# Performance work log

Measured on AMD Instinct MI355X. Metric: run time of the kernel, lower is better.

Reference implementation:

```python
import jax, jax.numpy as jnp
import numpy as np

NUM_LEVELS = 1000
DIMENSIONS = 10000


def setup_inputs() -> dict:
    key = jax.random.key(0)
    k1, k2, k3, k4 = jax.random.split(key, 4)
    x = jax.random.uniform(k1, (32, 1, 28, 28), dtype=jnp.float32)  # MNIST-like, values in [0,1)
    # torchhd Random / Level hypervectors are +/-1 (MAP VSA)
    pos_weight = jnp.where(jax.random.normal(k2, (784, DIMENSIONS)) > 0, 1.0, -1.0).astype(jnp.float32)
    level_weight = jnp.where(jax.random.normal(k3, (NUM_LEVELS, DIMENSIONS)) > 0, 1.0, -1.0).astype(jnp.float32)
    classify_weight = jax.random.normal(k4, (10, DIMENSIONS), dtype=jnp.float32) * 0.01
    return {"x": x, "pos_weight": pos_weight, "level_weight": level_weight,
            "classify_weight": classify_weight}


def reference(x, pos_weight, level_weight, classify_weight):
    B = x.shape[0]
    xf = x.reshape(B, -1)  # flatten -> [B, 784]
    # Level embedding: quantize value in [0,1] to nearest of NUM_LEVELS indices
    idx = jnp.clip(jnp.round(xf * (NUM_LEVELS - 1)), 0, NUM_LEVELS - 1).astype(jnp.int32)
    levels = jnp.take(level_weight, idx, axis=0)  # [B, 784, D] gather
    # bind (elementwise mult with position HVs) + multiset (sum over pixels)
    hv = jnp.einsum('pd,bpd->bd', pos_weight, levels)  # [B, D]
    # hard_quantize: sign with 0 -> -1
    enc = jnp.where(hv > 0, 1.0, -1.0).astype(hv.dtype)
    logit = enc @ classify_weight.T  # [B, num_classes]
    return logit
```

## Files before the change

### kernel.cpp

```cpp
#include <hip/hip_runtime.h>
#include <stdint.h>

#define D    10000
#define P    784
#define B    32
#define NL   1000
#define NC   10

#define ROWW 320
#define ROWB (ROWW * 4)
#define NW   313
#define CHUNKS 8
#define PLEN  98
#define PLANES 7

#define OFFS_OFF  0
#define LVL_OFF   (B * P * 4)
#define POS_OFF   (LVL_OFF + NL * ROWB)
#define PART_OFF  (POS_OFF + P * ROWB)

#define PACK_BPR 10

__global__ void k_pack(const float* __restrict__ x,
                       const float* __restrict__ lvl, const float* __restrict__ pos,
                       int* __restrict__ offs,
                       uint32_t* __restrict__ lvl_b, uint32_t* __restrict__ pos_b) {
    int bx  = blockIdx.x;
    int row = bx / PACK_BPR;
    int seg = bx % PACK_BPR;
    int d0  = seg * 1024 + threadIdx.x * 4;
    const float* src; uint32_t* dst;
    if (row < NL) { src = lvl + (size_t)row * D;        dst = lvl_b + (size_t)row * ROWW; }
    else          { src = pos + (size_t)(row - NL) * D; dst = pos_b + (size_t)(row - NL) * ROWW; }

    uint32_t nib = 0;
    if (d0 < D) {
        float4 v = *(const float4*)(src + d0);
        nib = (v.x < 0.0f ? 1u : 0u) | (v.y < 0.0f ? 2u : 0u) |
              (v.z < 0.0f ? 4u : 0u) | (v.w < 0.0f ? 8u : 0u);
    }
    int lane = threadIdx.x & 63;
    uint32_t val = nib << ((lane & 7) * 4);
    val |= __shfl_xor(val, 1, 64);
    val |= __shfl_xor(val, 2, 64);
    val |= __shfl_xor(val, 4, 64);
    if ((lane & 7) == 0) {
        int gword = (seg * 1024 + (threadIdx.x & ~7) * 4) >> 5;
        dst[gword] = val;
    }

    if (bx < 98) {
        int i = bx * 256 + threadIdx.x;
        float v = rintf(x[i] * 999.0f);
        v = fminf(fmaxf(v, 0.0f), 999.0f);
        offs[i] = (int)v * ROWB;
    }
}

__global__ __launch_bounds__(64) void k_bind(const int* __restrict__ offs,
                                             const uint32_t* __restrict__ lvl_b,
                                             const uint32_t* __restrict__ pos_b,
                                             uint32_t* __restrict__ part) {
    int b = blockIdx.z, c = blockIdx.y;
    int w = blockIdx.x * 64 + threadIdx.x;
    const int* po = offs + b * P + c * PLEN;
    const uint32_t* pb = pos_b + (size_t)(c * PLEN) * ROWW + w;
    const char* lb = (const char*)lvl_b;
    int wb = w << 2;

    uint32_t pl[PLANES];
    #pragma unroll
    for (int k = 0; k < PLANES; k++) pl[k] = 0;

    #pragma unroll 7
    for (int i = 0; i < PLEN; i += 2) {
        int o0 = po[i], o1 = po[i + 1];
        uint32_t l0 = *(const uint32_t*)(lb + o0 + wb);
        uint32_t l1 = *(const uint32_t*)(lb + o1 + wb);
        uint32_t x0 = l0 ^ pb[(size_t)i * ROWW];
        uint32_t x1 = l1 ^ pb[(size_t)(i + 1) * ROWW];
        uint32_t t  = x0 ^ x1;
        uint32_t cr = (x0 & x1) | (pl[0] & t);
        pl[0] ^= t;
        #pragma unroll
        for (int k = 1; k < PLANES; k++) { uint32_t tt = pl[k] & cr; pl[k] ^= cr; cr = tt; }
    }
    uint32_t* pp = part + (size_t)((b * CHUNKS + c) * PLANES) * ROWW + w;
    #pragma unroll
    for (int k = 0; k < PLANES; k++) pp[(size_t)k * ROWW] = pl[k];
}

template <int N>
__device__ inline void bsadd(const uint32_t* a, const uint32_t* b, uint32_t* s) {
    uint32_t cin = 0;
    #pragma unroll
    for (int k = 0; k < N; k++) {
        uint32_t t = a[k] ^ b[k];
        s[k] = t ^ cin;
        cin  = (a[k] & b[k]) | (cin & t);
    }
    s[N] = cin;
}

__global__ __launch_bounds__(320) void k_cls(const uint32_t* __restrict__ part,
                                             const float* __restrict__ cw,
                                             float* __restrict__ out) {
    int b = blockIdx.x;
    int w = threadIdx.x;
    float acc[NC];
    #pragma unroll
    for (int c = 0; c < NC; c++) acc[c] = 0.0f;

    if (w < NW) {
        uint32_t ch[CHUNKS][PLANES];
        #pragma unroll
        for (int c = 0; c < CHUNKS; c++)
            #pragma unroll
            for (int k = 0; k < PLANES; k++)
                ch[c][k] = part[(size_t)((b * CHUNKS + c) * PLANES + k) * ROWW + w];

        uint32_t s01[8], s23[8], s45[8], s67[8], t0[9], t1[9], s[10];
        bsadd<7>(ch[0], ch[1], s01);
        bsadd<7>(ch[2], ch[3], s23);
        bsadd<7>(ch[4], ch[5], s45);
        bsadd<7>(ch[6], ch[7], s67);
        bsadd<8>(s01, s23, t0);
        bsadd<8>(s45, s67, t1);
        bsadd<9>(t0, t1, s);
        uint32_t minus = s[9] | (s[8] & s[7] & (s[3] | s[4] | s[5] | s[6]));

        float sgn[32];
        #pragma unroll
        for (int j = 0; j < 32; j++) sgn[j] = ((minus >> j) & 1u) ? -1.0f : 1.0f;

        const float* wp = cw + w * 32;
        int lim = (w < NW - 1) ? 32 : 16;
        if (lim == 32) {
            #pragma unroll
            for (int c = 0; c < NC; c++) {
                const float* r = wp + c * D;
                float a = 0.0f;
                #pragma unroll
                for (int j = 0; j < 32; j++) a = fmaf(sgn[j], r[j], a);
                acc[c] = a;
            }
        } else {
            #pragma unroll
            for (int c = 0; c < NC; c++) {
                const float* r = wp + c * D;
                float a = 0.0f;
                #pragma unroll
                for (int j = 0; j < 16; j++) a = fmaf(sgn[j], r[j], a);
                acc[c] = a;
            }
        }
    }

    __shared__ float red[5][NC];
    int wave = threadIdx.x >> 6, lane = threadIdx.x & 63;
    #pragma unroll
    for (int c = 0; c < NC; c++) {
        float v = acc[c];
        for (int o = 32; o > 0; o >>= 1) v += __shfl_down(v, o, 64);
        if (lane == 0) red[wave][c] = v;
    }
    __syncthreads();
    if (threadIdx.x < NC) {
        float ssum = red[0][threadIdx.x] + red[1][threadIdx.x] + red[2][threadIdx.x]
                   + red[3][threadIdx.x] + red[4][threadIdx.x];
        out[b * NC + threadIdx.x] = ssum;
    }
}

extern "C" void kernel_launch(void* const* d_in, const int* in_sizes, int n_in,
                              void* d_out, int out_size, void* d_ws, size_t ws_size,
                              hipStream_t stream) {
    const float* x   = (const float*)d_in[0];
    const float* pos = (const float*)d_in[1];
    const float* lvl = (const float*)d_in[2];
    const float* cw  = (const float*)d_in[3];
    float* out = (float*)d_out;

    char* ws = (char*)d_ws;
    int*       offs  = (int*)(ws + OFFS_OFF);
    uint32_t*  lvl_b = (uint32_t*)(ws + LVL_OFF);
    uint32_t*  pos_b = (uint32_t*)(ws + POS_OFF);
    uint32_t*  part  = (uint32_t*)(ws + PART_OFF);

    k_pack<<<dim3((NL + P) * PACK_BPR), 256, 0, stream>>>(x, lvl, pos, offs, lvl_b, pos_b);
    k_bind<<<dim3(5, CHUNKS, B),         64, 0, stream>>>(offs, lvl_b, pos_b, part);
    k_cls <<<dim3(B),                   320, 0, stream>>>(part, cw, out);
}
```

Measured before the change: 127.7 us.

## Fuse bind and classify kernels, reduce chunks in LDS, atomically accumulate logits

Merges the bind and classify kernels into one launch. Each 512-thread block handles one batch element and a 64-word segment, with its 8 waves covering the 8 pixel chunks. Bit-plane partial counts are combined through shared memory instead of a global partial buffer, and each of 5 waves computes two class dot products that are added into the output with atomics. The output is zeroed in the pack kernel. This removes one launch and the global round trip of partial planes. In exchange, atomic float adds make the summation order nondeterministic, and the sign reduction is serialized in wave 0.

```diff
diff --git a/kernel.cpp b/kernel.cpp
--- a/kernel.cpp
+++ b/kernel.cpp
@@ -24,7 +24,8 @@
 __global__ void k_pack(const float* __restrict__ x,
                        const float* __restrict__ lvl, const float* __restrict__ pos,
                        int* __restrict__ offs,
-                       uint32_t* __restrict__ lvl_b, uint32_t* __restrict__ pos_b) {
+                       uint32_t* __restrict__ lvl_b, uint32_t* __restrict__ pos_b,
+                       float* __restrict__ out) {
     int bx  = blockIdx.x;
     int row = bx / PACK_BPR;
     int seg = bx % PACK_BPR;
@@ -55,18 +56,36 @@
         v = fminf(fmaxf(v, 0.0f), 999.0f);
         offs[i] = (int)v * ROWB;
     }
+    if (bx < 2) {
+        int i = bx * 256 + threadIdx.x;
+        if (i < B * NC) out[i] = 0.0f;
+    }
 }
 
-__global__ __launch_bounds__(64) void k_bind(const int* __restrict__ offs,
-                                             const uint32_t* __restrict__ lvl_b,
-                                             const uint32_t* __restrict__ pos_b,
-                                             uint32_t* __restrict__ part) {
-    int b = blockIdx.z, c = blockIdx.y;
-    int w = blockIdx.x * 64 + threadIdx.x;
-    const int* po = offs + b * P + c * PLEN;
-    const uint32_t* pb = pos_b + (size_t)(c * PLEN) * ROWW + w;
+template <int N>
+__device__ inline void bsadd(const uint32_t* a, const uint32_t* b, uint32_t* s) {
+    uint32_t cin = 0;
+    #pragma unroll
+    for (int k = 0; k < N; k++) {
+        uint32_t t = a[k] ^ b[k];
+        s[k] = t ^ cin;
+        cin  = (a[k] & b[k]) | (cin & t);
+    }
+    s[N] = cin;
+}
+
+__global__ __launch_bounds__(512) void k_bindcls(const int* __restrict__ offs,
+                                                 const uint32_t* __restrict__ lvl_b,
+                                                 const uint32_t* __restrict__ pos_b,
+                                                 const float* __restrict__ cw,
+                                                 float* __restrict__ out) {
+    int b = blockIdx.y, seg = blockIdx.x;
+    int wave = threadIdx.x >> 6, lane = threadIdx.x & 63;
+    int gw = seg * 64 + lane;
+    const int* po = offs + b * P + wave * PLEN;
+    const uint32_t* pb = pos_b + (size_t)(wave * PLEN) * ROWW + gw;
     const char* lb = (const char*)lvl_b;
-    int wb = w << 2;
+    int wb = gw << 2;
 
     uint32_t pl[PLANES];
     #pragma unroll
@@ -85,39 +104,20 @@
         #pragma unroll
         for (int k = 1; k < PLANES; k++) { uint32_t tt = pl[k] & cr; pl[k] ^= cr; cr = tt; }
     }
-    uint32_t* pp = part + (size_t)((b * CHUNKS + c) * PLANES) * ROWW + w;
+
+    __shared__ uint32_t red[CHUNKS][PLANES][64];
     #pragma unroll
-    for (int k = 0; k < PLANES; k++) pp[(size_t)k * ROWW] = pl[k];
-}
+    for (int k = 0; k < PLANES; k++) red[wave][k][lane] = pl[k];
+    __syncthreads();
 
-template <int N>
-__device__ inline void bsadd(const uint32_t* a, const uint32_t* b, uint32_t* s) {
-    uint32_t cin = 0;
-    #pragma unroll
-    for (int k = 0; k < N; k++) {
-        uint32_t t = a[k] ^ b[k];
-        s[k] = t ^ cin;
-        cin  = (a[k] & b[k]) | (cin & t);
-    }
-    s[N] = cin;
-}
-
-__global__ __launch_bounds__(320) void k_cls(const uint32_t* __restrict__ part,
-                                             const float* __restrict__ cw,
-                                             float* __restrict__ out) {
-    int b = blockIdx.x;
-    int w = threadIdx.x;
-    float acc[NC];
-    #pragma unroll
-    for (int c = 0; c < NC; c++) acc[c] = 0.0f;
-
-    if (w < NW) {
+    __shared__ uint32_t minus_s[64];
+    if (wave == 0) {
         uint32_t ch[CHUNKS][PLANES];
         #pragma unroll
         for (int c = 0; c < CHUNKS; c++)
             #pragma unroll
             for (int k = 0; k < PLANES; k++)
-                ch[c][k] = part[(size_t)((b * CHUNKS + c) * PLANES + k) * ROWW + w];
+                ch[c][k] = red[c][k][lane];
 
         uint32_t s01[8], s23[8], s45[8], s67[8], t0[9], t1[9], s[10];
         bsadd<7>(ch[0], ch[1], s01);
@@ -127,48 +127,32 @@
         bsadd<8>(s01, s23, t0);
         bsadd<8>(s45, s67, t1);
         bsadd<9>(t0, t1, s);
-        uint32_t minus = s[9] | (s[8] & s[7] & (s[3] | s[4] | s[5] | s[6]));
+        minus_s[lane] = s[9] | (s[8] & s[7] & (s[3] | s[4] | s[5] | s[6]));
+    }
+    __syncthreads();
 
+    if (wave < 5) {
+        uint32_t minus = minus_s[lane];
         float sgn[32];
         #pragma unroll
         for (int j = 0; j < 32; j++) sgn[j] = ((minus >> j) & 1u) ? -1.0f : 1.0f;
 
-        const float* wp = cw + w * 32;
-        int lim = (w < NW - 1) ? 32 : 16;
-        if (lim == 32) {
+        float a0 = 0.0f, a1 = 0.0f;
+        int c0 = wave * 2;
+        const float* r0 = cw + (size_t)c0 * D + gw * 32;
+        const float* r1 = r0 + D;
+        if (gw < NW - 1) {
             #pragma unroll
-            for (int c = 0; c < NC; c++) {
-                const float* r = wp + c * D;
-                float a = 0.0f;
-                #pragma unroll
-                for (int j = 0; j < 32; j++) a = fmaf(sgn[j], r[j], a);
-                acc[c] = a;
-            }
-        } else {
+            for (int j = 0; j < 32; j++) { a0 = fmaf(sgn[j], r0[j], a0); a1 = fmaf(sgn[j], r1[j], a1); }
+        } else if (gw == NW - 1) {
             #pragma unroll
-            for (int c = 0; c < NC; c++) {
-                const float* r = wp + c * D;
-                float a = 0.0f;
-                #pragma unroll
-                for (int j = 0; j < 16; j++) a = fmaf(sgn[j], r[j], a);
-                acc[c] = a;
-            }
+            for (int j = 0; j < 16; j++) { a0 = fmaf(sgn[j], r0[j], a0); a1 = fmaf(sgn[j], r1[j], a1); }
         }
-    }
-
-    __shared__ float red[5][NC];
-    int wave = threadIdx.x >> 6, lane = threadIdx.x & 63;
-    #pragma unroll
-    for (int c = 0; c < NC; c++) {
-        float v = acc[c];
-        for (int o = 32; o > 0; o >>= 1) v += __shfl_down(v, o, 64);
-        if (lane == 0) red[wave][c] = v;
-    }
-    __syncthreads();
-    if (threadIdx.x < NC) {
-        float ssum = red[0][threadIdx.x] + red[1][threadIdx.x] + red[2][threadIdx.x]
-                   + red[3][threadIdx.x] + red[4][threadIdx.x];
-        out[b * NC + threadIdx.x] = ssum;
+        for (int o = 32; o > 0; o >>= 1) { a0 += __shfl_down(a0, o, 64); a1 += __shfl_down(a1, o, 64); }
+        if (lane == 0) {
+            atomicAdd(out + b * NC + c0,     a0);
+            atomicAdd(out + b * NC + c0 + 1, a1);
+        }
     }
 }
 
@@ -185,9 +169,7 @@
     int*       offs  = (int*)(ws + OFFS_OFF);
     uint32_t*  lvl_b = (uint32_t*)(ws + LVL_OFF);
     uint32_t*  pos_b = (uint32_t*)(ws + POS_OFF);
-    uint32_t*  part  = (uint32_t*)(ws + PART_OFF);
 
-    k_pack<<<dim3((NL + P) * PACK_BPR), 256, 0, stream>>>(x, lvl, pos, offs, lvl_b, pos_b);
-    k_bind<<<dim3(5, CHUNKS, B),         64, 0, stream>>>(offs, lvl_b, pos_b, part);
-    k_cls <<<dim3(B),                   320, 0, stream>>>(part, cw, out);
+    k_pack   <<<dim3((NL + P) * PACK_BPR), 256, 0, stream>>>(x, lvl, pos, offs, lvl_b, pos_b, out);
+    k_bindcls<<<dim3(5, B),                512, 0, stream>>>(offs, lvl_b, pos_b, cw, out);
 }
```

Measured after the change: 114.9 us. 10.0% less time.
